# Kernel optimization log

Measured on AMD Instinct MI355X. Metric: run time of the kernel, lower is better.

Reference implementation:

```python
import jax, jax.numpy as jnp
import numpy as np


def setup_inputs() -> dict:
    key = jax.random.key(0)
    ks = jax.random.split(key, 7)
    B, D, T, H = 32, 512, 4096, 512
    return {
        "query": jax.random.normal(ks[0], (B, D, 1), dtype=jnp.float32),
        "keys": jax.random.normal(ks[1], (B, D, T), dtype=jnp.float32),
        "values": jax.random.normal(ks[2], (B, D, T), dtype=jnp.float32),
        "w42": 0.01 * jax.random.normal(ks[3], (H, 2 * D), dtype=jnp.float32),
        "b4": 0.01 * jax.random.normal(ks[4], (H, 1), dtype=jnp.float32),
        "w54": 0.01 * jax.random.normal(ks[5], (1, H), dtype=jnp.float32),
        "b5": 0.01 * jax.random.normal(ks[6], (1, 1), dtype=jnp.float32),
    }


def reference(query, keys, values, w42, b4, w54, b5):
    D = keys.shape[1]
    # cat([keys, query.repeat T], dim=1) then w42 @ cat ==
    # w42[:, :D] @ keys + w42[:, D:] @ query (broadcast over T)
    n4 = (jnp.einsum('hd,bdt->bht', w42[:, :D], keys)
          + jnp.einsum('hd,bdo->bho', w42[:, D:], query)  # [B,H,1], broadcasts over T
          + b4)                                            # [H,1] broadcasts
    a4 = jnp.tanh(n4)                                      # [B,H,T]
    n5 = jnp.einsum('oh,bht->bot', w54, a4) + b5           # [B,1,T]
    # transpose(1,2) -> [B,T,1], softmax over dim=1 (T)
    a5 = jax.nn.softmax(n5[:, 0, :], axis=-1)              # [B,T]
    a6 = jnp.einsum('bvt,bt->bv', values, a5)[..., None]   # [B,Dv,1]
    return a6
```

## Files before the change

kernel.cpp:

```cpp
#include <hip/hip_runtime.h>
#include <hip/hip_bf16.h>
#include <cstdint>
#include <cstddef>

typedef __attribute__((ext_vector_type(4))) float f32x4;
typedef __attribute__((ext_vector_type(8))) short s16x8;
typedef __attribute__((ext_vector_type(8))) unsigned short u16x8;

#define NB 32
#define DD 512
#define TT 4096
#define HH 512
#define NKK 16

__device__ __forceinline__ unsigned short f2bf(float f) {
  uint32_t u = __builtin_bit_cast(uint32_t, f);
  u += 0x7fffu + ((u >> 16) & 1u);
  return (unsigned short)(u >> 16);
}

__device__ __forceinline__ uint32_t cvtpk(float a, float b) {
  uint32_t d;
  asm("v_cvt_pk_bf16_f32 %0, %1, %2" : "=v"(d) : "v"(a), "v"(b));
  return d;
}

__device__ __forceinline__ float tanh_fast(float x) {
  x = fminf(fmaxf(x, -15.f), 15.f);
  float e = __expf(2.f * x);
  return (e - 1.f) / (e + 1.f);
}

__global__ void kConvT(const float* __restrict__ w42, u16x8* __restrict__ W1swz) {
  int g = blockIdx.x * 256 + threadIdx.x;
  int h = g & 511, sk = g >> 9;
  int kk = sk >> 2, s = sk & 3;
  const float* src = &w42[h * 1024 + kk * 32 + s * 8];
  f32x4 v0 = *reinterpret_cast<const f32x4*>(src);
  f32x4 v1 = *reinterpret_cast<const f32x4*>(src + 4);
  u16x8 c;
  c[0] = f2bf(v0.x); c[1] = f2bf(v0.y); c[2] = f2bf(v0.z); c[3] = f2bf(v0.w);
  c[4] = f2bf(v1.x); c[5] = f2bf(v1.y); c[6] = f2bf(v1.z); c[7] = f2bf(v1.w);
  W1swz[kk * 2048 + s * 512 + h] = c;
}

__global__ void kQterm(const float* __restrict__ w42, const float* __restrict__ query,
                       const float* __restrict__ b4, float* __restrict__ qterm) {
  int wid = blockIdx.x * 4 + (threadIdx.x >> 6);
  int lane = threadIdx.x & 63;
  int b = wid >> 9, h = wid & 511;
  const float* wr = &w42[h * 1024 + 512];
  const float* q  = &query[b * 512];
  int d = lane * 8;
  f32x4 w0 = *(const f32x4*)&wr[d], w1 = *(const f32x4*)&wr[d + 4];
  f32x4 q0 = *(const f32x4*)&q[d],  q1 = *(const f32x4*)&q[d + 4];
  float s = w0.x*q0.x + w0.y*q0.y + w0.z*q0.z + w0.w*q0.w
          + w1.x*q1.x + w1.y*q1.y + w1.z*q1.z + w1.w*q1.w;
  #pragma unroll
  for (int off = 32; off; off >>= 1) s += __shfl_xor(s, off);
  if (lane == 0) qterm[b * 512 + h] = s + b4[h];
}

__global__ __launch_bounds__(256, 2) void kGemmE(
    const float* __restrict__ keys, const u16x8* __restrict__ W1swz,
    const float* __restrict__ qterm, const float* __restrict__ w54,
    float* __restrict__ e, float* __restrict__ Zp) {
  __shared__ float red[4][64];

  int bid = blockIdx.x;
  int b = bid >> 6, tblk = bid & 63;
  int t0 = tblk * 64;
  int tid = threadIdx.x, lane = tid & 63, w = tid >> 6;
  int lr = lane & 15, lg = lane >> 4;

  const float* kb = keys + (size_t)b * DD * TT + (size_t)(lg * 8) * TT + t0 + lr;
  const s16x8* ap = reinterpret_cast<const s16x8*>(W1swz) + lg * 512 + w * 128 + lr;

  f32x4 acc[8][4];
  #pragma unroll
  for (int m = 0; m < 8; ++m)
    #pragma unroll
    for (int n = 0; n < 4; ++n) acc[m][n] = (f32x4){0.f, 0.f, 0.f, 0.f};

  s16x8 af[2][8];
  float rb[4][8];
  #pragma unroll
  for (int m = 0; m < 8; ++m) af[0][m] = ap[m * 16];
  #pragma unroll
  for (int n = 0; n < 4; ++n)
    #pragma unroll
    for (int j = 0; j < 8; ++j) rb[n][j] = kb[(size_t)j * TT + n * 16];

  #pragma unroll
  for (int kk = 0; kk < NKK; ++kk) {
    const int cur = kk & 1;
    s16x8 bf[4];
    #pragma unroll
    for (int n = 0; n < 4; ++n) {
      union { uint32_t u[4]; s16x8 v; } c;
      #pragma unroll
      for (int jj = 0; jj < 4; ++jj)
        c.u[jj] = cvtpk(rb[n][2 * jj], rb[n][2 * jj + 1]);
      bf[n] = c.v;
    }
    if (kk + 1 < NKK) {
      #pragma unroll
      for (int m = 0; m < 8; ++m) af[cur ^ 1][m] = ap[(kk + 1) * 2048 + m * 16];
      const float* kb2 = kb + (size_t)(kk + 1) * 32 * TT;
      #pragma unroll
      for (int n = 0; n < 4; ++n)
        #pragma unroll
        for (int j = 0; j < 8; ++j) rb[n][j] = kb2[(size_t)j * TT + n * 16];
    }
    #pragma unroll
    for (int m = 0; m < 8; ++m)
      #pragma unroll
      for (int n = 0; n < 4; ++n)
        acc[m][n] = __builtin_amdgcn_mfma_f32_16x16x32_bf16(af[cur][m], bf[n], acc[m][n], 0, 0, 0);
  }

  float part[4] = {0.f, 0.f, 0.f, 0.f};
  int hb = w * 128;
  #pragma unroll
  for (int m = 0; m < 8; ++m) {
    #pragma unroll
    for (int rr = 0; rr < 4; ++rr) {
      int h = hb + m * 16 + lg * 4 + rr;
      float qv = qterm[b * HH + h];
      float wv = w54[h];
      #pragma unroll
      for (int n = 0; n < 4; ++n)
        part[n] += wv * tanh_fast(acc[m][n][rr] + qv);
    }
  }
  #pragma unroll
  for (int n = 0; n < 4; ++n) {
    part[n] += __shfl_xor(part[n], 16);
    part[n] += __shfl_xor(part[n], 32);
  }
  if (lane < 16) {
    #pragma unroll
    for (int n = 0; n < 4; ++n) red[w][n * 16 + lane] = part[n];
  }
  __syncthreads();
  if (tid < 64) {
    float v = red[0][tid] + red[1][tid] + red[2][tid] + red[3][tid];
    float ev = __expf(v);
    e[b * TT + t0 + tid] = ev;
    float z = ev;
    #pragma unroll
    for (int off = 32; off; off >>= 1) z += __shfl_xor(z, off);
    if (tid == 0) Zp[b * 64 + tblk] = z;
  }
}

__global__ void kZinv(const float* __restrict__ Zp, float* __restrict__ Zinv) {
  int b = blockIdx.x, lane = threadIdx.x;
  float z = Zp[b * 64 + lane];
  #pragma unroll
  for (int off = 32; off; off >>= 1) z += __shfl_xor(z, off);
  if (lane == 0) Zinv[b] = 1.f / z;
}

__global__ void kOut(const float* __restrict__ values, const float* __restrict__ e,
                     const float* __restrict__ Zinv, float* __restrict__ out) {
  int blk = blockIdx.x;
  int b = blk >> 7;
  int wid = threadIdx.x >> 6, lane = threadIdx.x & 63;
  int v = (blk & 127) * 4 + wid;
  const float* row = &values[((size_t)b * 512 + v) * TT];
  const float* wv = &e[b * TT];
  float s0 = 0.f, s1 = 0.f, s2 = 0.f, s3 = 0.f;
  #pragma unroll
  for (int i = 0; i < 16; ++i) {
    int t = (i * 64 + lane) * 4;
    f32x4 x = __builtin_nontemporal_load(reinterpret_cast<const f32x4*>(&row[t]));
    f32x4 y = *(const f32x4*)&wv[t];
    float d = x.x * y.x + x.y * y.y + x.z * y.z + x.w * y.w;
    if ((i & 3) == 0) s0 += d; else if ((i & 3) == 1) s1 += d;
    else if ((i & 3) == 2) s2 += d; else s3 += d;
  }
  float s = (s0 + s1) + (s2 + s3);
  #pragma unroll
  for (int off = 32; off; off >>= 1) s += __shfl_xor(s, off);
  if (lane == 0) out[b * 512 + v] = s * Zinv[b];
}

extern "C" void kernel_launch(void* const* d_in, const int* in_sizes, int n_in,
                              void* d_out, int out_size, void* d_ws, size_t ws_size,
                              hipStream_t stream) {
  const float* query  = (const float*)d_in[0];
  const float* keys   = (const float*)d_in[1];
  const float* values = (const float*)d_in[2];
  const float* w42    = (const float*)d_in[3];
  const float* b4     = (const float*)d_in[4];
  const float* w54    = (const float*)d_in[5];
  float* out = (float*)d_out;

  char* ws = (char*)d_ws;
  u16x8* W1swz = (u16x8*)ws;
  float* qterm = (float*)(ws + (512 << 10));
  float* Zp    = (float*)(ws + (576 << 10));
  float* Zinv  = (float*)(ws + (592 << 10));
  float* e     = (float*)(ws + (640 << 10));

  kConvT <<<128, 256, 0, stream>>>(w42, W1swz);
  kQterm <<<4096, 256, 0, stream>>>(w42, query, b4, qterm);
  kGemmE <<<2048, 256, 0, stream>>>(keys, W1swz, qterm, w54, e, Zp);
  kZinv  <<<32, 64, 0, stream>>>(Zp, Zinv);
  kOut   <<<4096, 256, 0, stream>>>(values, e, Zinv, out);
}
```

Baseline: 190.2 us.

## Stage keys tile through swizzled LDS with vectorized loads and two-deep prefetch

Before, each wave loaded its own scalar key elements straight from global memory, so every wave fetched the full 64-column keys tile and each lane issued 32 strided scalar loads per k-step. Now the block cooperatively loads each keys slice once with 16-byte nontemporal vector loads, converts it to bf16 pairs and writes it to an XOR-swizzled double-buffered LDS tile. Waves then read MFMA B fragments from LDS after a barrier. Register and weight prefetch is now two k-steps deep. This cuts redundant global traffic and scalar load count, at the cost of a barrier per k-step and extra LDS reads.

```diff
diff --git a/kernel.cpp b/kernel.cpp
--- a/kernel.cpp
+++ b/kernel.cpp
@@ -65,6 +65,7 @@
     const float* __restrict__ keys, const u16x8* __restrict__ W1swz,
     const float* __restrict__ qterm, const float* __restrict__ w54,
     float* __restrict__ e, float* __restrict__ Zp) {
+  __shared__ s16x8 Bs[2][256];
   __shared__ float red[4][64];
 
   int bid = blockIdx.x;
@@ -73,8 +74,18 @@
   int tid = threadIdx.x, lane = tid & 63, w = tid >> 6;
   int lr = lane & 15, lg = lane >> 4;
 
-  const float* kb = keys + (size_t)b * DD * TT + (size_t)(lg * 8) * TT + t0 + lr;
+  int p = tid >> 4, tg = tid & 15;
+  const float* kp0 = keys + (size_t)b * DD * TT + (size_t)(2 * p) * TT + t0 + tg * 4;
+  const float* kp1 = kp0 + TT;
+  int wsl = p * 16 + (tg ^ p);
   const s16x8* ap = reinterpret_cast<const s16x8*>(W1swz) + lg * 512 + w * 128 + lr;
+  int base2[4];
+  #pragma unroll
+  for (int pp = 0; pp < 4; ++pp) {
+    int pq = lg * 4 + pp;
+    int q0 = lr >> 2;
+    base2[pp] = (pq * 64 + (q0 ^ (pq & 3)) * 4 + (lr & 3)) ^ (lg << 4);
+  }
 
   f32x4 acc[8][4];
   #pragma unroll
@@ -83,40 +94,50 @@
     for (int n = 0; n < 4; ++n) acc[m][n] = (f32x4){0.f, 0.f, 0.f, 0.f};
 
   s16x8 af[2][8];
-  float rb[4][8];
+  f32x4 rb[2][2];
   #pragma unroll
   for (int m = 0; m < 8; ++m) af[0][m] = ap[m * 16];
-  #pragma unroll
-  for (int n = 0; n < 4; ++n)
-    #pragma unroll
-    for (int j = 0; j < 8; ++j) rb[n][j] = kb[(size_t)j * TT + n * 16];
+  rb[0][0] = __builtin_nontemporal_load(reinterpret_cast<const f32x4*>(kp0));
+  rb[0][1] = __builtin_nontemporal_load(reinterpret_cast<const f32x4*>(kp1));
+  #pragma unroll
+  for (int m = 0; m < 8; ++m) af[1][m] = ap[2048 + m * 16];
+  rb[1][0] = __builtin_nontemporal_load(reinterpret_cast<const f32x4*>(kp0 + (size_t)32 * TT));
+  rb[1][1] = __builtin_nontemporal_load(reinterpret_cast<const f32x4*>(kp1 + (size_t)32 * TT));
 
   #pragma unroll
   for (int kk = 0; kk < NKK; ++kk) {
     const int cur = kk & 1;
+    union { uint32_t q[4]; s16x8 v; } c;
+    #pragma unroll
+    for (int dt = 0; dt < 4; ++dt) c.q[dt] = cvtpk(rb[cur][0][dt], rb[cur][1][dt]);
+    Bs[cur][wsl] = c.v;
+    if (kk + 2 < NKK) {
+      rb[cur][0] = __builtin_nontemporal_load(
+          reinterpret_cast<const f32x4*>(kp0 + (size_t)(kk + 2) * 32 * TT));
+      rb[cur][1] = __builtin_nontemporal_load(
+          reinterpret_cast<const f32x4*>(kp1 + (size_t)(kk + 2) * 32 * TT));
+    }
+    asm volatile("s_waitcnt lgkmcnt(0)" ::: "memory");
+    __builtin_amdgcn_s_barrier();
+
+    const uint32_t* B32 = reinterpret_cast<const uint32_t*>(&Bs[cur][0]);
     s16x8 bf[4];
     #pragma unroll
     for (int n = 0; n < 4; ++n) {
-      union { uint32_t u[4]; s16x8 v; } c;
-      #pragma unroll
-      for (int jj = 0; jj < 4; ++jj)
-        c.u[jj] = cvtpk(rb[n][2 * jj], rb[n][2 * jj + 1]);
-      bf[n] = c.v;
-    }
-    if (kk + 1 < NKK) {
-      #pragma unroll
-      for (int m = 0; m < 8; ++m) af[cur ^ 1][m] = ap[(kk + 1) * 2048 + m * 16];
-      const float* kb2 = kb + (size_t)(kk + 1) * 32 * TT;
-      #pragma unroll
-      for (int n = 0; n < 4; ++n)
-        #pragma unroll
-        for (int j = 0; j < 8; ++j) rb[n][j] = kb2[(size_t)j * TT + n * 16];
+      union { uint32_t q[4]; s16x8 v; } bb;
+      #pragma unroll
+      for (int pp = 0; pp < 4; ++pp) bb.q[pp] = B32[base2[pp] ^ (n * 16)];
+      bf[n] = bb.v;
     }
     #pragma unroll
     for (int m = 0; m < 8; ++m)
       #pragma unroll
       for (int n = 0; n < 4; ++n)
         acc[m][n] = __builtin_amdgcn_mfma_f32_16x16x32_bf16(af[cur][m], bf[n], acc[m][n], 0, 0, 0);
+    if (kk + 2 < NKK) {
+      #pragma unroll
+      for (int m = 0; m < 8; ++m) af[cur][m] = ap[(kk + 2) * 2048 + m * 16];
+    }
   }
 
   float part[4] = {0.f, 0.f, 0.f, 0.f};
```

After: 183.7 us. 3.4% less time.
